# Kernel optimization log

Hardware: AMD Instinct MI355X
Metric: run time of the kernel (lower is better)

## Reference

```python
import jax, jax.numpy as jnp
import numpy as np

Q_DEFAULT = 8
XI_MAX = 0.4          # center frequency of the highest-frequency wavelet (cycles/sample)
BW_RATIO = 0.8        # bandwidth-to-center-frequency ratio
LOG_EPS = 1e-6


def _make_filters(T, Q):
    """Morlet-style analytic filter bank in the Fourier domain (all static numpy)."""
    J = int(np.floor(np.log2(T / 2)))
    freqs = np.fft.fftfreq(T).astype(np.float32)          # [T], in [-0.5, 0.5)
    # first-order wavelets: J*Q filters, geometrically spaced, quality factor Q
    n1 = J * Q
    xi1 = (XI_MAX * 2.0 ** (-np.arange(n1) / Q)).astype(np.float32)
    sig1 = (BW_RATIO * xi1 / Q).astype(np.float32)
    psi1 = np.exp(-(freqs[None, :] - xi1[:, None]) ** 2 / (2.0 * sig1[:, None] ** 2)).astype(np.float32)  # [n1, T]
    # second-order wavelets: Q2 = 1, one per octave
    xi2 = (XI_MAX * 2.0 ** (-np.arange(J))).astype(np.float32)
    sig2 = (BW_RATIO * xi2).astype(np.float32)
    psi2 = np.exp(-(freqs[None, :] - xi2[:, None]) ** 2 / (2.0 * sig2[:, None] ** 2)).astype(np.float32)  # [J, T]
    # low-pass (phi): Gaussian at scale 2^J
    sigma_phi = np.float32(BW_RATIO * XI_MAX * 2.0 ** (-J))
    phi = np.exp(-(freqs ** 2) / (2.0 * sigma_phi ** 2)).astype(np.float32)  # [T]
    # valid second-order paths: xi2 strictly below xi1 (frequency-decreasing cascade)
    pair_j1, pair_k = [], []
    for k in range(J):
        for j1 in range(n1):
            if xi2[k] < xi1[j1]:
                pair_j1.append(j1)
                pair_k.append(k)
    return psi1, psi2, phi, np.asarray(pair_j1, np.int32), np.asarray(pair_k, np.int32)


def _scatter(x_flat, psi1, psi2, phi, pair_j1, pair_k):
    """x_flat: [N, T] real. Returns S: [N, 1 + n1 + n_pairs, T]."""
    xh = jnp.fft.fft(x_flat)                                   # [N, T] complex
    S0 = jnp.fft.ifft(xh * phi).real[:, None, :]               # order 0 (dropped later)
    U1 = jnp.abs(jnp.fft.ifft(xh[:, None, :] * psi1[None]))    # [N, n1, T]
    U1h = jnp.fft.fft(U1)
    S1 = jnp.fft.ifft(U1h * phi).real                          # [N, n1, T]
    U2 = jnp.abs(jnp.fft.ifft(U1h[:, pair_j1, :] * psi2[pair_k][None]))  # [N, P, T]
    S2 = jnp.fft.ifft(jnp.fft.fft(U2) * phi).real              # [N, P, T]
    return jnp.concatenate([S0, S1, S2], axis=1)


def setup_inputs() -> dict:
    key = jax.random.key(0)
    x = jax.random.normal(key, (8, 2048, 6), dtype=jnp.float32)
    return {"x": x}


def reference(x):
    B, T, C = x.shape
    psi1, psi2, phi, pj, pk = _make_filters(T, Q_DEFAULT)
    psi1, psi2, phi = jnp.asarray(psi1), jnp.asarray(psi2), jnp.asarray(phi)
    # vectorize the original per-channel Python loop: fold channels into batch
    xf = jnp.transpose(x, (0, 2, 1)).reshape(B * C, T)          # [B*C, T]
    S = _scatter(xf, psi1, psi2, phi, pj, pk)                   # [B*C, n_coef+1, T]
    out = jnp.mean(jnp.log(S[:, 1:, :] + LOG_EPS), axis=-1)     # drop order-0, log, time-mean
    return out.reshape(B, C, -1).transpose(0, 2, 1)             # [B, n_coef, C]
```

## Files before the change

kernel.cpp:

```cpp
#include <hip/hip_runtime.h>

#define NTH 256
#define U1H_STRIDE 21504

#define PHI1 0.29504296f
#define PHI2 0.0075683594f
#define GCUT 18.0f

__device__ __forceinline__ int swz(int i) { return i ^ (((i >> 4) & 3) * 5); }

__device__ __forceinline__ float2 cmul(float2 a, float2 b) {
  return make_float2(a.x * b.x - a.y * b.y, a.x * b.y + a.y * b.x);
}

template <int W>
__device__ __forceinline__ float wsum(float v) {
#pragma unroll
  for (int off = 1; off < W; off <<= 1) v += __shfl_xor(v, off, 64);
  return v;
}

template <int M>
__device__ __forceinline__ int prevM(int i) {
  if (M == 128)
    return ((i >> 5) & 3) | (((i >> 3) & 3) << 2) | (((i >> 1) & 3) << 4) | ((i & 1) << 6);
  else if (M == 256)
    return ((i & 3) << 6) | (((i >> 2) & 3) << 4) | (((i >> 4) & 3) << 2) | ((i >> 6) & 3);
  else if (M == 512)
    return ((i >> 7) & 3) | (((i >> 5) & 3) << 2) | (((i >> 3) & 3) << 4) |
           (((i >> 1) & 3) << 6) | ((i & 1) << 8);
  else if (M == 1024)
    return ((i >> 8) & 3) | (((i >> 6) & 3) << 2) | (((i >> 4) & 3) << 4) |
           (((i >> 2) & 3) << 6) | ((i & 3) << 8);
  else
    return ((i >> 9) & 3) | (((i >> 7) & 3) << 2) | (((i >> 5) & 3) << 4) |
           (((i >> 3) & 3) << 6) | (((i >> 1) & 3) << 8) | ((i & 1) << 10);
}

template <bool INV>
__device__ __forceinline__ void dif4(float2* A, int j, int ls, float astep) {
  const int s = 1 << ls;
  const int e = j & (s - 1);
  const int base = ((j >> ls) << (ls + 2)) | e;
  float2 w1;
  __sincosf(astep * (float)e, &w1.y, &w1.x);
  if (INV) w1.y = -w1.y;
  const float2 w2 = cmul(w1, w1);
  const float2 w3 = cmul(w2, w1);
  const float2 a0 = A[swz(base)];
  const float2 a1 = A[swz(base + s)];
  const float2 a2 = A[swz(base + 2 * s)];
  const float2 a3 = A[swz(base + 3 * s)];
  const float t0x = a0.x + a2.x, t0y = a0.y + a2.y;
  const float t1x = a0.x - a2.x, t1y = a0.y - a2.y;
  const float t2x = a1.x + a3.x, t2y = a1.y + a3.y;
  const float bdx = a1.x - a3.x, bdy = a1.y - a3.y;
  const float sgn = INV ? -1.0f : 1.0f;
  const float t3x = sgn * bdy, t3y = -sgn * bdx;
  A[swz(base)]         = make_float2(t0x + t2x, t0y + t2y);
  A[swz(base + s)]     = cmul(make_float2(t1x + t3x, t1y + t3y), w1);
  A[swz(base + 2 * s)] = cmul(make_float2(t0x - t2x, t0y - t2y), w2);
  A[swz(base + 3 * s)] = cmul(make_float2(t1x - t3x, t1y - t3y), w3);
}

__device__ __forceinline__ void dit4(float2* A, int j, int ls, float astep) {
  const int s = 1 << ls;
  const int e = j & (s - 1);
  const int base = ((j >> ls) << (ls + 2)) | e;
  float2 w1;
  __sincosf(astep * (float)e, &w1.y, &w1.x);
  const float2 w2 = cmul(w1, w1);
  const float2 w3 = cmul(w2, w1);
  const float2 c0 = A[swz(base)];
  const float2 c1 = cmul(A[swz(base + s)], w1);
  const float2 c2 = cmul(A[swz(base + 2 * s)], w2);
  const float2 c3 = cmul(A[swz(base + 3 * s)], w3);
  const float t0x = c0.x + c2.x, t0y = c0.y + c2.y;
  const float t1x = c0.x - c2.x, t1y = c0.y - c2.y;
  const float t2x = c1.x + c3.x, t2y = c1.y + c3.y;
  const float bdx = c1.x - c3.x, bdy = c1.y - c3.y;
  const float t3x = bdy, t3y = -bdx;
  A[swz(base)]         = make_float2(t0x + t2x, t0y + t2y);
  A[swz(base + s)]     = make_float2(t1x + t3x, t1y + t3y);
  A[swz(base + 2 * s)] = make_float2(t0x - t2x, t0y - t2y);
  A[swz(base + 3 * s)] = make_float2(t1x - t3x, t1y - t3y);
}

__device__ __forceinline__ void r2pair(float2* A, int g) {
  const float2 a = A[swz(2 * g)];
  const float2 b = A[swz(2 * g + 1)];
  A[swz(2 * g)]     = make_float2(a.x + b.x, a.y + b.y);
  A[swz(2 * g + 1)] = make_float2(a.x - b.x, a.y - b.y);
}

template <int M> struct LMof { static constexpr int v =
  (M == 2048) ? 11 : (M == 1024) ? 10 : (M == 512) ? 9 : (M == 256) ? 8 : 7; };

template <int M, bool INV>
__device__ __forceinline__ void dif_blk(float2* A) {
  constexpr int LM = LMof<M>::v;
  constexpr int NB = M / 4;
  const int tid = (int)threadIdx.x;
#pragma unroll
  for (int ls = LM - 2; ls >= (LM & 1); ls -= 2) {
    const float astep = -1.5707963267948966f / (float)(1 << ls);
    __syncthreads();
#pragma unroll
    for (int i = 0; i < NB / NTH; ++i) dif4<INV>(A, tid + NTH * i, ls, astep);
  }
  if (LM & 1) {
    __syncthreads();
#pragma unroll
    for (int i = 0; i < (M / 2) / NTH; ++i) r2pair(A, tid + NTH * i);
  }
  __syncthreads();
}

template <int M>
__device__ __forceinline__ void dit_blk(float2* A) {
  constexpr int LM = LMof<M>::v;
  constexpr int NB = M / 4;
  const int tid = (int)threadIdx.x;
  if (LM & 1) {
    __syncthreads();
#pragma unroll
    for (int i = 0; i < (M / 2) / NTH; ++i) r2pair(A, tid + NTH * i);
  }
#pragma unroll
  for (int ls = (LM & 1); ls <= LM - 2; ls += 2) {
    const float astep = -1.5707963267948966f / (float)(1 << ls);
    __syncthreads();
#pragma unroll
    for (int i = 0; i < NB / NTH; ++i) dit4(A, tid + NTH * i, ls, astep);
  }
  __syncthreads();
}

template <int M, bool INV, int LANES>
__device__ __forceinline__ void dif_w(float2* Aw, int l) {
  constexpr int LM = LMof<M>::v;
  constexpr int NB = M / 4;
#pragma unroll
  for (int ls = LM - 2; ls >= (LM & 1); ls -= 2) {
    const float astep = -1.5707963267948966f / (float)(1 << ls);
#pragma unroll
    for (int i = 0; i < NB / LANES; ++i) dif4<INV>(Aw, l + LANES * i, ls, astep);
  }
  if (LM & 1) {
#pragma unroll
    for (int i = 0; i < (M / 2) / LANES; ++i) r2pair(Aw, l + LANES * i);
  }
}

template <int M, int LANES>
__device__ __forceinline__ void dit_w(float2* Aw, int l) {
  constexpr int LM = LMof<M>::v;
  constexpr int NB = M / 4;
  if (LM & 1) {
#pragma unroll
    for (int i = 0; i < (M / 2) / LANES; ++i) r2pair(Aw, l + LANES * i);
  }
#pragma unroll
  for (int ls = (LM & 1); ls <= LM - 2; ls += 2) {
    const float astep = -1.5707963267948966f / (float)(1 << ls);
#pragma unroll
    for (int i = 0; i < NB / LANES; ++i) dit4(Aw, l + LANES * i, ls, astep);
  }
}

__device__ __forceinline__ int u1h_off(int j1) {
  const int o = j1 >> 3;
  if (o == 0) return j1 * 1024;
  if (o == 1) return 8192 + (j1 - 8) * 512;
  if (o == 2) return 12288 + (j1 - 16) * 256;
  return 14336 + (j1 - 24) * 128;
}

__global__ __launch_bounds__(NTH) void kA(const float* __restrict__ x,
                                          float2* __restrict__ xh) {
  __shared__ float2 A[2048];
  const int n = blockIdx.x, b = n / 6, c = n % 6;
  const float* xp = x + (size_t)b * (2048 * 6) + c;
#pragma unroll
  for (int i = 0; i < 8; ++i) {
    const int t = (int)threadIdx.x + NTH * i;
    A[swz(t)] = make_float2(xp[t * 6], 0.0f);
  }
  dif_blk<2048, false>(A);
#pragma unroll
  for (int i = 0; i < 8; ++i) {
    const int t = (int)threadIdx.x + NTH * i;
    xh[(size_t)n * 2048 + prevM<2048>(t)] = A[swz(t)];
  }
}

template <int M1>
__device__ __forceinline__ void kB_blk(float2* A, const float2* __restrict__ src,
                                       float2* __restrict__ U1h, float* __restrict__ out,
                                       int n, int b, int c, int j1) {
  constexpr int F = 2048 / M1;
  constexpr int NR = M1 / NTH;
  const int tid = (int)threadIdx.x;
  const float xi = 0.4f * exp2f(-0.125f * (float)j1);
  const float sig = 0.1f * xi;
  const float i2s = 1.0f / (2.0f * sig * sig);
#pragma unroll
  for (int i = 0; i < NR; ++i) {
    const int m = tid + NTH * i;
    float2 acc = make_float2(0.0f, 0.0f);
#pragma unroll
    for (int q = 0; q < F; ++q) {
      const int f = m + q * M1;
      const float fr = (float)(f < 1024 ? f : f - 2048) * (1.0f / 2048.0f);
      const float d = fr - xi;
      const float dd = d * d * i2s;
      if (dd < GCUT) {
        const float g = __expf(-dd);
        const float2 v = src[f];
        acc.x += v.x * g; acc.y += v.y * g;
      }
    }
    A[swz(m)] = acc;
  }
  dif_blk<M1, true>(A);
#pragma unroll
  for (int i = 0; i < NR; ++i) {
    const int m = tid + NTH * i;
    const float2 zv = A[swz(m)];
    A[swz(m)] = make_float2(sqrtf(zv.x * zv.x + zv.y * zv.y) * (1.0f / 2048.0f), 0.0f);
  }
  dit_blk<M1>(A);
  float2* dst = U1h + (size_t)n * U1H_STRIDE + u1h_off(j1);
#pragma unroll
  for (int i = 0; i < NR; ++i) {
    const int m = tid + NTH * i;
    dst[m] = A[swz(m)];
  }
  const float invM = 1.0f / (float)M1;
  const float c0 = A[0].x * invM;
  const float2 U1 = A[1], U2 = A[2];
  __syncthreads();
  const float k1 = PHI1 * 2.0f * invM, k2 = PHI2 * 2.0f * invM;
  float part = 0.0f;
#pragma unroll
  for (int i = 0; i < NR; ++i) {
    const int t = tid + NTH * i;
    float sv, cv;
    __sincosf((6.283185307179586f / (float)M1) * (float)t, &sv, &cv);
    float acc = c0 + k1 * (U1.x * cv - U1.y * sv);
    const float c2 = cv * cv - sv * sv, s2 = 2.0f * sv * cv;
    acc += k2 * (U2.x * c2 - U2.y * s2);
    part += __logf(acc + 1e-6f);
  }
  part = wsum<64>(part);
  float* scr = (float*)A;
  const int lane = tid & 63, wid = tid >> 6;
  if (lane == 0) scr[wid] = part;
  __syncthreads();
  if (tid == 0)
    out[((size_t)b * 440 + j1) * 6 + c] = (scr[0] + scr[1] + scr[2] + scr[3]) * invM;
}

template <int M1>
__device__ __forceinline__ void kB_wav(float2* A, const float2* __restrict__ src,
                                       float2* __restrict__ U1h, float* __restrict__ out,
                                       int n, int b, int c, int j1base) {
  constexpr int NRW = M1 / 64;
  constexpr int F = 2048 / M1;
  const int tid = (int)threadIdx.x;
  const int l = tid & 63, wid = tid >> 6;
  const int j1 = j1base + wid;
  float2* Aw = A + wid * M1;
  const float xi = 0.4f * exp2f(-0.125f * (float)j1);
  const float sig = 0.1f * xi;
  const float i2s = 1.0f / (2.0f * sig * sig);
#pragma unroll
  for (int i = 0; i < NRW; ++i) {
    const int m = l + 64 * i;
    float2 acc = make_float2(0.0f, 0.0f);
#pragma unroll
    for (int q = 0; q < F; ++q) {
      const int f = m + q * M1;
      const float fr = (float)(f < 1024 ? f : f - 2048) * (1.0f / 2048.0f);
      const float d = fr - xi;
      const float dd = d * d * i2s;
      if (dd < GCUT) {
        const float g = __expf(-dd);
        const float2 v = src[f];
        acc.x += v.x * g; acc.y += v.y * g;
      }
    }
    Aw[swz(m)] = acc;
  }
  dif_w<M1, true, 64>(Aw, l);
#pragma unroll
  for (int i = 0; i < NRW; ++i) {
    const int m = l + 64 * i;
    const float2 zv = Aw[swz(m)];
    Aw[swz(m)] = make_float2(sqrtf(zv.x * zv.x + zv.y * zv.y) * (1.0f / 2048.0f), 0.0f);
  }
  dit_w<M1, 64>(Aw, l);
  float2* dst = U1h + (size_t)n * U1H_STRIDE + u1h_off(j1);
#pragma unroll
  for (int i = 0; i < NRW; ++i) {
    const int m = l + 64 * i;
    dst[m] = Aw[swz(m)];
  }
  const float invM = 1.0f / (float)M1;
  const float c0 = Aw[0].x * invM;
  const float2 U1 = Aw[1], U2 = Aw[2];
  const float k1 = PHI1 * 2.0f * invM, k2 = PHI2 * 2.0f * invM;
  float part = 0.0f;
#pragma unroll
  for (int i = 0; i < NRW; ++i) {
    const int t = l + 64 * i;
    float sv, cv;
    __sincosf((6.283185307179586f / (float)M1) * (float)t, &sv, &cv);
    float acc = c0 + k1 * (U1.x * cv - U1.y * sv);
    const float c2 = cv * cv - sv * sv, s2 = 2.0f * sv * cv;
    acc += k2 * (U2.x * c2 - U2.y * s2);
    part += __logf(acc + 1e-6f);
  }
  part = wsum<64>(part);
  if (l == 0) out[((size_t)b * 440 + j1) * 6 + c] = part * invM;
}

__device__ __forceinline__ void kB_dual(float2* A, const float2* __restrict__ src,
                                        float2* __restrict__ U1h, float* __restrict__ out,
                                        int n, int b, int c, int j1base) {
  const int tid = (int)threadIdx.x;
  const int l = tid & 63, wid = tid >> 6;
  const int h = l >> 5, ll = l & 31;
  const int j1 = j1base + 2 * wid + h;
  float2* Ah = A + wid * 256 + h * 128;
  const float xi = 0.4f * exp2f(-0.125f * (float)j1);
  const float sig = 0.1f * xi;
  const float i2s = 1.0f / (2.0f * sig * sig);
#pragma unroll
  for (int i = 0; i < 4; ++i) {
    const int m = ll + 32 * i;
    float2 acc = make_float2(0.0f, 0.0f);
#pragma unroll
    for (int q = 0; q < 16; ++q) {
      const int f = m + q * 128;
      const float fr = (float)(f < 1024 ? f : f - 2048) * (1.0f / 2048.0f);
      const float d = fr - xi;
      const float dd = d * d * i2s;
      if (dd < GCUT) {
        const float g = __expf(-dd);
        const float2 v = src[f];
        acc.x += v.x * g; acc.y += v.y * g;
      }
    }
    Ah[swz(m)] = acc;
  }
  dif_w<128, true, 32>(Ah, ll);
#pragma unroll
  for (int i = 0; i < 4; ++i) {
    const int m = ll + 32 * i;
    const float2 zv = Ah[swz(m)];
    Ah[swz(m)] = make_float2(sqrtf(zv.x * zv.x + zv.y * zv.y) * (1.0f / 2048.0f), 0.0f);
  }
  dit_w<128, 32>(Ah, ll);
  float2* dst = U1h + (size_t)n * U1H_STRIDE + u1h_off(j1);
#pragma unroll
  for (int i = 0; i < 4; ++i) {
    const int m = ll + 32 * i;
    dst[m] = Ah[swz(m)];
  }
  const float invM = 1.0f / 128.0f;
  const float c0 = Ah[0].x * invM;
  const float2 U1 = Ah[1], U2 = Ah[2];
  const float k1 = PHI1 * 2.0f * invM, k2 = PHI2 * 2.0f * invM;
  float part = 0.0f;
#pragma unroll
  for (int i = 0; i < 4; ++i) {
    const int t = ll + 32 * i;
    float sv, cv;
    __sincosf((6.283185307179586f / 128.0f) * (float)t, &sv, &cv);
    float acc = c0 + k1 * (U1.x * cv - U1.y * sv);
    const float c2 = cv * cv - sv * sv, s2 = 2.0f * sv * cv;
    acc += k2 * (U2.x * c2 - U2.y * s2);
    part += __logf(acc + 1e-6f);
  }
  part = wsum<32>(part);
  if (ll == 0) out[((size_t)b * 440 + j1) * 6 + c] = part * invM;
}

__global__ __launch_bounds__(NTH, 8) void kB_all(const float2* __restrict__ xh,
                                                 float2* __restrict__ U1h,
                                                 float* __restrict__ out) {
  __shared__ float2 A[2048];
  const int ci = (int)blockIdx.x / 48;
  const int n  = (int)blockIdx.x % 48;
  const int b = n / 6, c = n % 6;
  const float2* src = xh + (size_t)n * 2048;
  if (ci < 2)       kB_wav<512>(A, src, U1h, out, n, b, c, 8 + 4 * ci);
  else if (ci < 10) kB_blk<1024>(A, src, U1h, out, n, b, c, ci - 2);
  else if (ci < 12) kB_wav<256>(A, src, U1h, out, n, b, c, 16 + 4 * (ci - 10));
  else              kB_dual(A, src, U1h, out, n, b, c, 24 + 8 * (ci - 12));
}

template <int M2>
__device__ __forceinline__ void kC_blk(float2* A, const float2* __restrict__ V,
                                       float* __restrict__ outp, int M1, int F, float xi) {
  constexpr int NR2 = M2 / NTH;
  const int tid = (int)threadIdx.x;
  const float sg = 0.8f * xi;
  const float i2s = 1.0f / (2.0f * sg * sg);
#pragma unroll
  for (int ii = 0; ii < NR2; ++ii) {
    const int m = tid + NTH * ii;
    float2 acc = make_float2(0.0f, 0.0f);
    for (int q = 0; q < F; ++q) {
      const int f = m + q * M2;
      const float fr = (float)(f < (M1 >> 1) ? f : f - M1) * (1.0f / 2048.0f);
      const float d = fr - xi;
      const float dd = d * d * i2s;
      if (dd < GCUT) {
        const float g = __expf(-dd);
        const float2 vv = V[f];
        acc.x += vv.x * g; acc.y += vv.y * g;
      }
    }
    A[swz(m)] = acc;
  }
  dif_blk<M2, true>(A);
  const float invM1f = 1.0f / (float)M1;
  float b0 = 0, b1r = 0, b1i = 0, b2r = 0, b2i = 0;
#pragma unroll
  for (int ii = 0; ii < NR2; ++ii) {
    const int idx = tid + NTH * ii;
    const float2 zv = A[swz(idx)];
    const float u = sqrtf(zv.x * zv.x + zv.y * zv.y) * invM1f;
    const int t = prevM<M2>(idx);
    float sv, cv;
    __sincosf((6.283185307179586f / (float)M2) * (float)t, &sv, &cv);
    b0 += u;
    b1r += u * cv; b1i -= u * sv;
    const float c2 = cv * cv - sv * sv, s2 = 2.0f * sv * cv;
    b2r += u * c2; b2i -= u * s2;
  }
  b0 = wsum<64>(b0);
  b1r = wsum<64>(b1r); b1i = wsum<64>(b1i);
  b2r = wsum<64>(b2r); b2i = wsum<64>(b2i);
  __syncthreads();
  float* scr = (float*)A;
  const int lane = tid & 63, wid = tid >> 6;
  if (lane == 0) {
    scr[wid * 5 + 0] = b0;
    scr[wid * 5 + 1] = b1r; scr[wid * 5 + 2] = b1i;
    scr[wid * 5 + 3] = b2r; scr[wid * 5 + 4] = b2i;
  }
  __syncthreads();
  float Bv[5];
#pragma unroll
  for (int bi = 0; bi < 5; ++bi)
    Bv[bi] = scr[bi] + scr[5 + bi] + scr[10 + bi] + scr[15 + bi];
  const float k1 = 2.0f * PHI1, k2 = 2.0f * PHI2;
  const float invM2 = 1.0f / (float)M2;
  float part = 0.0f;
#pragma unroll
  for (int ii = 0; ii < NR2; ++ii) {
    const int idx = tid + NTH * ii;
    const int t = prevM<M2>(idx);
    float sv, cv;
    __sincosf((6.283185307179586f / (float)M2) * (float)t, &sv, &cv);
    float acc = Bv[0] + k1 * (Bv[1] * cv - Bv[2] * sv);
    const float c2 = cv * cv - sv * sv, s2 = 2.0f * sv * cv;
    acc += k2 * (Bv[3] * c2 - Bv[4] * s2);
    part += __logf(acc * invM2 + 1e-6f);
  }
  part = wsum<64>(part);
  if (lane == 0) scr[20 + wid] = part;
  __syncthreads();
  if (tid == 0)
    *outp = (scr[20] + scr[21] + scr[22] + scr[23]) * invM2;
}

template <int M2>
__device__ __forceinline__ void kC_wav(float2* Aw, const float2* __restrict__ V,
                                       float* __restrict__ outp, int M1, int F,
                                       float xi, int l) {
  constexpr int NR2 = M2 / 64;
  const float sg = 0.8f * xi;
  const float i2s = 1.0f / (2.0f * sg * sg);
#pragma unroll
  for (int ii = 0; ii < NR2; ++ii) {
    const int m = l + 64 * ii;
    float2 acc = make_float2(0.0f, 0.0f);
    for (int q = 0; q < F; ++q) {
      const int f = m + q * M2;
      const float fr = (float)(f < (M1 >> 1) ? f : f - M1) * (1.0f / 2048.0f);
      const float d = fr - xi;
      const float dd = d * d * i2s;
      if (dd < GCUT) {
        const float g = __expf(-dd);
        const float2 vv = V[f];
        acc.x += vv.x * g; acc.y += vv.y * g;
      }
    }
    Aw[swz(m)] = acc;
  }
  dif_w<M2, true, 64>(Aw, l);
  const float invM1f = 1.0f / (float)M1;
  float cvs[NR2], svs[NR2];
  float b0 = 0, b1r = 0, b1i = 0, b2r = 0, b2i = 0;
#pragma unroll
  for (int ii = 0; ii < NR2; ++ii) {
    const int idx = l + 64 * ii;
    const float2 zv = Aw[swz(idx)];
    const float u = sqrtf(zv.x * zv.x + zv.y * zv.y) * invM1f;
    const int t = prevM<M2>(idx);
    float sv, cv;
    __sincosf((6.283185307179586f / (float)M2) * (float)t, &sv, &cv);
    cvs[ii] = cv; svs[ii] = sv;
    b0 += u;
    b1r += u * cv; b1i -= u * sv;
    const float c2 = cv * cv - sv * sv, s2 = 2.0f * sv * cv;
    b2r += u * c2; b2i -= u * s2;
  }
  b0 = wsum<64>(b0);
  b1r = wsum<64>(b1r); b1i = wsum<64>(b1i);
  b2r = wsum<64>(b2r); b2i = wsum<64>(b2i);
  const float k1 = 2.0f * PHI1, k2 = 2.0f * PHI2;
  const float invM2 = 1.0f / (float)M2;
  float part = 0.0f;
#pragma unroll
  for (int ii = 0; ii < NR2; ++ii) {
    const float cv = cvs[ii], sv = svs[ii];
    float acc = b0 + k1 * (b1r * cv - b1i * sv);
    const float c2 = cv * cv - sv * sv, s2 = 2.0f * sv * cv;
    acc += k2 * (b2r * c2 - b2i * s2);
    part += __logf(acc * invM2 + 1e-6f);
  }
  part = wsum<64>(part);
  if (l == 0) *outp = part * invM2;
}

__device__ __forceinline__ void kC_dual(float2* Ah, const float2* __restrict__ V,
                                        float* __restrict__ outp, int M1, int F,
                                        float xi, int ll) {
  const float sg = 0.8f * xi;
  const float i2s = 1.0f / (2.0f * sg * sg);
#pragma unroll
  for (int ii = 0; ii < 4; ++ii) {
    const int m = ll + 32 * ii;
    float2 acc = make_float2(0.0f, 0.0f);
    for (int q = 0; q < F; ++q) {
      const int f = m + q * 128;
      const float fr = (float)(f < (M1 >> 1) ? f : f - M1) * (1.0f / 2048.0f);
      const float d = fr - xi;
      const float dd = d * d * i2s;
      if (dd < GCUT) {
        const float g = __expf(-dd);
        const float2 vv = V[f];
        acc.x += vv.x * g; acc.y += vv.y * g;
      }
    }
    Ah[swz(m)] = acc;
  }
  dif_w<128, true, 32>(Ah, ll);
  const float invM1f = 1.0f / (float)M1;
  float cvs[4], svs[4];
  float b0 = 0, b1r = 0, b1i = 0, b2r = 0, b2i = 0;
#pragma unroll
  for (int ii = 0; ii < 4; ++ii) {
    const int idx = ll + 32 * ii;
    const float2 zv = Ah[swz(idx)];
    const float u = sqrtf(zv.x * zv.x + zv.y * zv.y) * invM1f;
    const int t = prevM<128>(idx);
    float sv, cv;
    __sincosf((6.283185307179586f / 128.0f) * (float)t, &sv, &cv);
    cvs[ii] = cv; svs[ii] = sv;
    b0 += u;
    b1r += u * cv; b1i -= u * sv;
    const float c2 = cv * cv - sv * sv, s2 = 2.0f * sv * cv;
    b2r += u * c2; b2i -= u * s2;
  }
  b0 = wsum<32>(b0);
  b1r = wsum<32>(b1r); b1i = wsum<32>(b1i);
  b2r = wsum<32>(b2r); b2i = wsum<32>(b2i);
  const float k1 = 2.0f * PHI1, k2 = 2.0f * PHI2;
  const float invM2 = 1.0f / 128.0f;
  float part = 0.0f;
#pragma unroll
  for (int ii = 0; ii < 4; ++ii) {
    const float cv = cvs[ii], sv = svs[ii];
    float acc = b0 + k1 * (b1r * cv - b1i * sv);
    const float c2 = cv * cv - sv * sv, s2 = 2.0f * sv * cv;
    acc += k2 * (b2r * c2 - b2i * s2);
    part += __logf(acc * invM2 + 1e-6f);
  }
  part = wsum<32>(part);
  if (ll == 0) *outp = part * invM2;
}

__global__ __launch_bounds__(NTH, 8) void kC_all(const float2* __restrict__ U1h,
                                                 float* __restrict__ out) {
  __shared__ float2 A[2048];
  const int ci = (int)blockIdx.x / 48;
  const int n  = (int)blockIdx.x % 48;
  const int b = n / 6, c = n % 6;
  const float2* base = U1h + (size_t)n * U1H_STRIDE;
  const int wid = (int)threadIdx.x >> 6;
  const int l = (int)threadIdx.x & 63;
  if (ci < 4) {
    const int k = 2;
    const int j1 = 4 * ci + wid;
    const int M1 = (j1 < 8) ? 1024 : 512;
    const float xi = 0.4f * exp2f(-(float)k);
    const int p = 4 * k * (k - 1) + j1;
    kC_wav<512>(A + wid * 512, base + u1h_off(j1),
                out + ((size_t)b * 440 + 80 + p) * 6 + c, M1, M1 / 512, xi, l);
  } else if (ci < 6) {
    const int k = 3;
    const int j1 = 4 * (ci - 4) + wid;
    const float xi = 0.4f * exp2f(-(float)k);
    const int p = 4 * k * (k - 1) + j1;
    kC_wav<512>(A + wid * 512, base + u1h_off(j1),
                out + ((size_t)b * 440 + 80 + p) * 6 + c, 1024, 2, xi, l);
  } else if (ci < 14) {
    const int k = 1;
    const int j1 = ci - 6;
    const float xi = 0.4f * exp2f(-(float)k);
    const int p = 4 * k * (k - 1) + j1;
    kC_blk<1024>(A, base + u1h_off(j1), out + ((size_t)b * 440 + 80 + p) * 6 + c,
                 1024, 1, xi);
  } else if (ci < 18) {
    const int k = 3;
    const int j1 = 8 + 4 * (ci - 14) + wid;
    const int M1 = (j1 < 16) ? 512 : 256;
    const float xi = 0.4f * exp2f(-(float)k);
    const int p = 4 * k * (k - 1) + j1;
    kC_wav<256>(A + wid * 256, base + u1h_off(j1),
                out + ((size_t)b * 440 + 80 + p) * 6 + c, M1, M1 / 256, xi, l);
  } else if (ci < 20) {
    const int k = 4;
    const int j1 = 4 * (ci - 18) + wid;
    const float xi = 0.4f * exp2f(-(float)k);
    const int p = 4 * k * (k - 1) + j1;
    kC_wav<256>(A + wid * 256, base + u1h_off(j1),
                out + ((size_t)b * 440 + 80 + p) * 6 + c, 1024, 4, xi, l);
  } else if (ci < 23) {
    const int k = 4;
    const int h = l >> 5, ll = l & 31;
    const int j1 = 8 + 8 * (ci - 20) + 2 * wid + h;
    const int o = j1 >> 3;
    const int M1 = (o < 3) ? (1024 >> o) : 128;
    const float xi = 0.4f * exp2f(-(float)k);
    const int p = 4 * k * (k - 1) + j1;
    kC_dual(A + wid * 256 + h * 128, base + u1h_off(j1),
            out + ((size_t)b * 440 + 80 + p) * 6 + c, M1, M1 / 128, xi, ll);
  } else {
    int g = ci - 23;
    int k = 5;
    while (g >= k) { g -= k; ++k; }
    const int h = l >> 5, ll = l & 31;
    const int j1 = 8 * g + 2 * wid + h;
    const int M1 = (g < 3) ? (1024 >> g) : 128;
    const float xi = 0.4f * exp2f(-(float)k);
    const int p = 4 * k * (k - 1) + j1;
    kC_dual(A + wid * 256 + h * 128, base + u1h_off(j1),
            out + ((size_t)b * 440 + 80 + p) * 6 + c, M1, M1 / 128, xi, ll);
  }
}

extern "C" void kernel_launch(void* const* d_in, const int* in_sizes, int n_in,
                              void* d_out, int out_size, void* d_ws, size_t ws_size,
                              hipStream_t stream) {
  (void)in_sizes; (void)n_in; (void)out_size; (void)ws_size;
  const float* x = (const float*)d_in[0];
  float* out = (float*)d_out;
  float2* U1h = (float2*)d_ws;
  float2* xh = (float2*)((char*)d_ws + (size_t)48 * U1H_STRIDE * sizeof(float2));
  kA<<<dim3(48), dim3(NTH), 0, stream>>>(x, xh);
  kB_all<<<dim3(19 * 48), dim3(NTH), 0, stream>>>(xh, U1h, out);
  kC_all<<<dim3(58 * 48), dim3(NTH), 0, stream>>>(U1h, out);
}
```

Measured before the change: 96.70 us.

## Fuse first- and second-order scattering kernels, keep U1 spectrum in LDS

Merges the first-order (kB) and second-order (kC) kernels into one kernel. Each block computes a parent first-order wavelet spectrum in shared memory and then evaluates all of its descendant second-order paths directly from that shared-memory copy. This removes the global U1h workspace round trip and one kernel launch. In exchange the per-block shared-memory footprint doubles, launch bounds drop to 4 blocks per CU, the grid shrinks from 58*48 to 19*48 blocks, and per-block work becomes uneven. Parallelism and load balance may suffer.

```diff
diff --git a/kernel.cpp b/kernel.cpp
--- a/kernel.cpp
+++ b/kernel.cpp
@@ -1,7 +1,6 @@
 #include <hip/hip_runtime.h>
 
 #define NTH 256
-#define U1H_STRIDE 21504
 
 #define PHI1 0.29504296f
 #define PHI2 0.0075683594f
@@ -168,14 +167,6 @@
   }
 }
 
-__device__ __forceinline__ int u1h_off(int j1) {
-  const int o = j1 >> 3;
-  if (o == 0) return j1 * 1024;
-  if (o == 1) return 8192 + (j1 - 8) * 512;
-  if (o == 2) return 12288 + (j1 - 16) * 256;
-  return 14336 + (j1 - 24) * 128;
-}
-
 __global__ __launch_bounds__(NTH) void kA(const float* __restrict__ x,
                                           float2* __restrict__ xh) {
   __shared__ float2 A[2048];
@@ -194,12 +185,13 @@
   }
 }
 
-template <int M1>
-__device__ __forceinline__ void kB_blk(float2* A, const float2* __restrict__ src,
-                                       float2* __restrict__ U1h, float* __restrict__ out,
-                                       int n, int b, int c, int j1) {
-  constexpr int F = 2048 / M1;
-  constexpr int NR = M1 / NTH;
+
+__device__ __forceinline__ void parent_blk1024(float2* A, float* scr,
+                                               const float2* __restrict__ src,
+                                               float* __restrict__ out,
+                                               int b, int c, int j1) {
+  constexpr int M1 = 1024;
+  constexpr int NR = 4;
   const int tid = (int)threadIdx.x;
   const float xi = 0.4f * exp2f(-0.125f * (float)j1);
   const float sig = 0.1f * xi;
@@ -207,6 +199,64 @@
 #pragma unroll
   for (int i = 0; i < NR; ++i) {
     const int m = tid + NTH * i;
+    float2 acc = make_float2(0.0f, 0.0f);
+#pragma unroll
+    for (int q = 0; q < 2; ++q) {
+      const int f = m + q * M1;
+      const float fr = (float)(f < 1024 ? f : f - 2048) * (1.0f / 2048.0f);
+      const float d = fr - xi;
+      const float dd = d * d * i2s;
+      if (dd < GCUT) {
+        const float g = __expf(-dd);
+        const float2 v = src[f];
+        acc.x += v.x * g; acc.y += v.y * g;
+      }
+    }
+    A[swz(m)] = acc;
+  }
+  dif_blk<M1, true>(A);
+#pragma unroll
+  for (int i = 0; i < NR; ++i) {
+    const int m = tid + NTH * i;
+    const float2 zv = A[swz(m)];
+    A[swz(m)] = make_float2(sqrtf(zv.x * zv.x + zv.y * zv.y) * (1.0f / 2048.0f), 0.0f);
+  }
+  dit_blk<M1>(A);
+  const float invM = 1.0f / (float)M1;
+  const float c0 = A[0].x * invM;
+  const float2 U1 = A[1], U2 = A[2];
+  const float k1 = PHI1 * 2.0f * invM, k2 = PHI2 * 2.0f * invM;
+  float part = 0.0f;
+#pragma unroll
+  for (int i = 0; i < NR; ++i) {
+    const int t = tid + NTH * i;
+    float sv, cv;
+    __sincosf((6.283185307179586f / (float)M1) * (float)t, &sv, &cv);
+    float acc = c0 + k1 * (U1.x * cv - U1.y * sv);
+    const float c2 = cv * cv - sv * sv, s2 = 2.0f * sv * cv;
+    acc += k2 * (U2.x * c2 - U2.y * s2);
+    part += __logf(acc + 1e-6f);
+  }
+  part = wsum<64>(part);
+  const int lane = tid & 63, wid = tid >> 6;
+  if (lane == 0) scr[wid] = part;
+  __syncthreads();
+  if (tid == 0)
+    out[((size_t)b * 440 + j1) * 6 + c] = (scr[0] + scr[1] + scr[2] + scr[3]) * invM;
+}
+
+template <int M1>
+__device__ __forceinline__ void parent_wav(float2* Aw, const float2* __restrict__ src,
+                                           float* __restrict__ out,
+                                           int b, int c, int j1, int l) {
+  constexpr int NRW = M1 / 64;
+  constexpr int F = 2048 / M1;
+  const float xi = 0.4f * exp2f(-0.125f * (float)j1);
+  const float sig = 0.1f * xi;
+  const float i2s = 1.0f / (2.0f * sig * sig);
+#pragma unroll
+  for (int i = 0; i < NRW; ++i) {
+    const int m = l + 64 * i;
     float2 acc = make_float2(0.0f, 0.0f);
 #pragma unroll
     for (int q = 0; q < F; ++q) {
@@ -220,76 +270,6 @@
         acc.x += v.x * g; acc.y += v.y * g;
       }
     }
-    A[swz(m)] = acc;
-  }
-  dif_blk<M1, true>(A);
-#pragma unroll
-  for (int i = 0; i < NR; ++i) {
-    const int m = tid + NTH * i;
-    const float2 zv = A[swz(m)];
-    A[swz(m)] = make_float2(sqrtf(zv.x * zv.x + zv.y * zv.y) * (1.0f / 2048.0f), 0.0f);
-  }
-  dit_blk<M1>(A);
-  float2* dst = U1h + (size_t)n * U1H_STRIDE + u1h_off(j1);
-#pragma unroll
-  for (int i = 0; i < NR; ++i) {
-    const int m = tid + NTH * i;
-    dst[m] = A[swz(m)];
-  }
-  const float invM = 1.0f / (float)M1;
-  const float c0 = A[0].x * invM;
-  const float2 U1 = A[1], U2 = A[2];
-  __syncthreads();
-  const float k1 = PHI1 * 2.0f * invM, k2 = PHI2 * 2.0f * invM;
-  float part = 0.0f;
-#pragma unroll
-  for (int i = 0; i < NR; ++i) {
-    const int t = tid + NTH * i;
-    float sv, cv;
-    __sincosf((6.283185307179586f / (float)M1) * (float)t, &sv, &cv);
-    float acc = c0 + k1 * (U1.x * cv - U1.y * sv);
-    const float c2 = cv * cv - sv * sv, s2 = 2.0f * sv * cv;
-    acc += k2 * (U2.x * c2 - U2.y * s2);
-    part += __logf(acc + 1e-6f);
-  }
-  part = wsum<64>(part);
-  float* scr = (float*)A;
-  const int lane = tid & 63, wid = tid >> 6;
-  if (lane == 0) scr[wid] = part;
-  __syncthreads();
-  if (tid == 0)
-    out[((size_t)b * 440 + j1) * 6 + c] = (scr[0] + scr[1] + scr[2] + scr[3]) * invM;
-}
-
-template <int M1>
-__device__ __forceinline__ void kB_wav(float2* A, const float2* __restrict__ src,
-                                       float2* __restrict__ U1h, float* __restrict__ out,
-                                       int n, int b, int c, int j1base) {
-  constexpr int NRW = M1 / 64;
-  constexpr int F = 2048 / M1;
-  const int tid = (int)threadIdx.x;
-  const int l = tid & 63, wid = tid >> 6;
-  const int j1 = j1base + wid;
-  float2* Aw = A + wid * M1;
-  const float xi = 0.4f * exp2f(-0.125f * (float)j1);
-  const float sig = 0.1f * xi;
-  const float i2s = 1.0f / (2.0f * sig * sig);
-#pragma unroll
-  for (int i = 0; i < NRW; ++i) {
-    const int m = l + 64 * i;
-    float2 acc = make_float2(0.0f, 0.0f);
-#pragma unroll
-    for (int q = 0; q < F; ++q) {
-      const int f = m + q * M1;
-      const float fr = (float)(f < 1024 ? f : f - 2048) * (1.0f / 2048.0f);
-      const float d = fr - xi;
-      const float dd = d * d * i2s;
-      if (dd < GCUT) {
-        const float g = __expf(-dd);
-        const float2 v = src[f];
-        acc.x += v.x * g; acc.y += v.y * g;
-      }
-    }
     Aw[swz(m)] = acc;
   }
   dif_w<M1, true, 64>(Aw, l);
@@ -300,12 +280,6 @@
     Aw[swz(m)] = make_float2(sqrtf(zv.x * zv.x + zv.y * zv.y) * (1.0f / 2048.0f), 0.0f);
   }
   dit_w<M1, 64>(Aw, l);
-  float2* dst = U1h + (size_t)n * U1H_STRIDE + u1h_off(j1);
-#pragma unroll
-  for (int i = 0; i < NRW; ++i) {
-    const int m = l + 64 * i;
-    dst[m] = Aw[swz(m)];
-  }
   const float invM = 1.0f / (float)M1;
   const float c0 = Aw[0].x * invM;
   const float2 U1 = Aw[1], U2 = Aw[2];
@@ -325,14 +299,9 @@
   if (l == 0) out[((size_t)b * 440 + j1) * 6 + c] = part * invM;
 }
 
-__device__ __forceinline__ void kB_dual(float2* A, const float2* __restrict__ src,
-                                        float2* __restrict__ U1h, float* __restrict__ out,
-                                        int n, int b, int c, int j1base) {
-  const int tid = (int)threadIdx.x;
-  const int l = tid & 63, wid = tid >> 6;
-  const int h = l >> 5, ll = l & 31;
-  const int j1 = j1base + 2 * wid + h;
-  float2* Ah = A + wid * 256 + h * 128;
+__device__ __forceinline__ void parent_dual(float2* Ah, const float2* __restrict__ src,
+                                            float* __restrict__ out,
+                                            int b, int c, int j1, int ll) {
   const float xi = 0.4f * exp2f(-0.125f * (float)j1);
   const float sig = 0.1f * xi;
   const float i2s = 1.0f / (2.0f * sig * sig);
@@ -362,12 +331,6 @@
     Ah[swz(m)] = make_float2(sqrtf(zv.x * zv.x + zv.y * zv.y) * (1.0f / 2048.0f), 0.0f);
   }
   dit_w<128, 32>(Ah, ll);
-  float2* dst = U1h + (size_t)n * U1H_STRIDE + u1h_off(j1);
-#pragma unroll
-  for (int i = 0; i < 4; ++i) {
-    const int m = ll + 32 * i;
-    dst[m] = Ah[swz(m)];
-  }
   const float invM = 1.0f / 128.0f;
   const float c0 = Ah[0].x * invM;
   const float2 U1 = Ah[1], U2 = Ah[2];
@@ -387,101 +350,10 @@
   if (ll == 0) out[((size_t)b * 440 + j1) * 6 + c] = part * invM;
 }
 
-__global__ __launch_bounds__(NTH, 8) void kB_all(const float2* __restrict__ xh,
-                                                 float2* __restrict__ U1h,
-                                                 float* __restrict__ out) {
-  __shared__ float2 A[2048];
-  const int ci = (int)blockIdx.x / 48;
-  const int n  = (int)blockIdx.x % 48;
-  const int b = n / 6, c = n % 6;
-  const float2* src = xh + (size_t)n * 2048;
-  if (ci < 2)       kB_wav<512>(A, src, U1h, out, n, b, c, 8 + 4 * ci);
-  else if (ci < 10) kB_blk<1024>(A, src, U1h, out, n, b, c, ci - 2);
-  else if (ci < 12) kB_wav<256>(A, src, U1h, out, n, b, c, 16 + 4 * (ci - 10));
-  else              kB_dual(A, src, U1h, out, n, b, c, 24 + 8 * (ci - 12));
-}
-
 template <int M2>
-__device__ __forceinline__ void kC_blk(float2* A, const float2* __restrict__ V,
-                                       float* __restrict__ outp, int M1, int F, float xi) {
-  constexpr int NR2 = M2 / NTH;
-  const int tid = (int)threadIdx.x;
-  const float sg = 0.8f * xi;
-  const float i2s = 1.0f / (2.0f * sg * sg);
-#pragma unroll
-  for (int ii = 0; ii < NR2; ++ii) {
-    const int m = tid + NTH * ii;
-    float2 acc = make_float2(0.0f, 0.0f);
-    for (int q = 0; q < F; ++q) {
-      const int f = m + q * M2;
-      const float fr = (float)(f < (M1 >> 1) ? f : f - M1) * (1.0f / 2048.0f);
-      const float d = fr - xi;
-      const float dd = d * d * i2s;
-      if (dd < GCUT) {
-        const float g = __expf(-dd);
-        const float2 vv = V[f];
-        acc.x += vv.x * g; acc.y += vv.y * g;
-      }
-    }
-    A[swz(m)] = acc;
-  }
-  dif_blk<M2, true>(A);
-  const float invM1f = 1.0f / (float)M1;
-  float b0 = 0, b1r = 0, b1i = 0, b2r = 0, b2i = 0;
-#pragma unroll
-  for (int ii = 0; ii < NR2; ++ii) {
-    const int idx = tid + NTH * ii;
-    const float2 zv = A[swz(idx)];
-    const float u = sqrtf(zv.x * zv.x + zv.y * zv.y) * invM1f;
-    const int t = prevM<M2>(idx);
-    float sv, cv;
-    __sincosf((6.283185307179586f / (float)M2) * (float)t, &sv, &cv);
-    b0 += u;
-    b1r += u * cv; b1i -= u * sv;
-    const float c2 = cv * cv - sv * sv, s2 = 2.0f * sv * cv;
-    b2r += u * c2; b2i -= u * s2;
-  }
-  b0 = wsum<64>(b0);
-  b1r = wsum<64>(b1r); b1i = wsum<64>(b1i);
-  b2r = wsum<64>(b2r); b2i = wsum<64>(b2i);
-  __syncthreads();
-  float* scr = (float*)A;
-  const int lane = tid & 63, wid = tid >> 6;
-  if (lane == 0) {
-    scr[wid * 5 + 0] = b0;
-    scr[wid * 5 + 1] = b1r; scr[wid * 5 + 2] = b1i;
-    scr[wid * 5 + 3] = b2r; scr[wid * 5 + 4] = b2i;
-  }
-  __syncthreads();
-  float Bv[5];
-#pragma unroll
-  for (int bi = 0; bi < 5; ++bi)
-    Bv[bi] = scr[bi] + scr[5 + bi] + scr[10 + bi] + scr[15 + bi];
-  const float k1 = 2.0f * PHI1, k2 = 2.0f * PHI2;
-  const float invM2 = 1.0f / (float)M2;
-  float part = 0.0f;
-#pragma unroll
-  for (int ii = 0; ii < NR2; ++ii) {
-    const int idx = tid + NTH * ii;
-    const int t = prevM<M2>(idx);
-    float sv, cv;
-    __sincosf((6.283185307179586f / (float)M2) * (float)t, &sv, &cv);
-    float acc = Bv[0] + k1 * (Bv[1] * cv - Bv[2] * sv);
-    const float c2 = cv * cv - sv * sv, s2 = 2.0f * sv * cv;
-    acc += k2 * (Bv[3] * c2 - Bv[4] * s2);
-    part += __logf(acc * invM2 + 1e-6f);
-  }
-  part = wsum<64>(part);
-  if (lane == 0) scr[20 + wid] = part;
-  __syncthreads();
-  if (tid == 0)
-    *outp = (scr[20] + scr[21] + scr[22] + scr[23]) * invM2;
-}
-
-template <int M2>
-__device__ __forceinline__ void kC_wav(float2* Aw, const float2* __restrict__ V,
-                                       float* __restrict__ outp, int M1, int F,
-                                       float xi, int l) {
+__device__ __forceinline__ void desc_wav(float2* Aw, const float2* __restrict__ Vl,
+                                         float* __restrict__ outp, int M1, int F,
+                                         float xi, int l) {
   constexpr int NR2 = M2 / 64;
   const float sg = 0.8f * xi;
   const float i2s = 1.0f / (2.0f * sg * sg);
@@ -496,7 +368,7 @@
       const float dd = d * d * i2s;
       if (dd < GCUT) {
         const float g = __expf(-dd);
-        const float2 vv = V[f];
+        const float2 vv = Vl[swz(f)];
         acc.x += vv.x * g; acc.y += vv.y * g;
       }
     }
@@ -538,9 +410,9 @@
   if (l == 0) *outp = part * invM2;
 }
 
-__device__ __forceinline__ void kC_dual(float2* Ah, const float2* __restrict__ V,
-                                        float* __restrict__ outp, int M1, int F,
-                                        float xi, int ll) {
+__device__ __forceinline__ void desc_dual(float2* Ah, const float2* __restrict__ Vl,
+                                          float* __restrict__ outp, int M1, int F,
+                                          float xi, int ll) {
   const float sg = 0.8f * xi;
   const float i2s = 1.0f / (2.0f * sg * sg);
 #pragma unroll
@@ -554,7 +426,7 @@
       const float dd = d * d * i2s;
       if (dd < GCUT) {
         const float g = __expf(-dd);
-        const float2 vv = V[f];
+        const float2 vv = Vl[swz(f)];
         acc.x += vv.x * g; acc.y += vv.y * g;
       }
     }
@@ -596,73 +468,72 @@
   if (ll == 0) *outp = part * invM2;
 }
 
-__global__ __launch_bounds__(NTH, 8) void kC_all(const float2* __restrict__ U1h,
-                                                 float* __restrict__ out) {
-  __shared__ float2 A[2048];
+__device__ __forceinline__ float* o2p(float* out, int b, int c, int j1, int k) {
+  return out + ((size_t)b * 440 + 80 + 4 * k * (k - 1) + j1) * 6 + c;
+}
+__device__ __forceinline__ float xi2f(int k) { return 0.4f * exp2f(-(float)k); }
+
+__global__ __launch_bounds__(NTH, 4) void kBC(const float2* __restrict__ xh,
+                                              float* __restrict__ out) {
+  __shared__ float2 L[4096];
   const int ci = (int)blockIdx.x / 48;
   const int n  = (int)blockIdx.x % 48;
   const int b = n / 6, c = n % 6;
-  const float2* base = U1h + (size_t)n * U1H_STRIDE;
-  const int wid = (int)threadIdx.x >> 6;
-  const int l = (int)threadIdx.x & 63;
-  if (ci < 4) {
-    const int k = 2;
-    const int j1 = 4 * ci + wid;
-    const int M1 = (j1 < 8) ? 1024 : 512;
-    const float xi = 0.4f * exp2f(-(float)k);
-    const int p = 4 * k * (k - 1) + j1;
-    kC_wav<512>(A + wid * 512, base + u1h_off(j1),
-                out + ((size_t)b * 440 + 80 + p) * 6 + c, M1, M1 / 512, xi, l);
-  } else if (ci < 6) {
-    const int k = 3;
-    const int j1 = 4 * (ci - 4) + wid;
-    const float xi = 0.4f * exp2f(-(float)k);
-    const int p = 4 * k * (k - 1) + j1;
-    kC_wav<512>(A + wid * 512, base + u1h_off(j1),
-                out + ((size_t)b * 440 + 80 + p) * 6 + c, 1024, 2, xi, l);
-  } else if (ci < 14) {
-    const int k = 1;
-    const int j1 = ci - 6;
-    const float xi = 0.4f * exp2f(-(float)k);
-    const int p = 4 * k * (k - 1) + j1;
-    kC_blk<1024>(A, base + u1h_off(j1), out + ((size_t)b * 440 + 80 + p) * 6 + c,
-                 1024, 1, xi);
-  } else if (ci < 18) {
-    const int k = 3;
-    const int j1 = 8 + 4 * (ci - 14) + wid;
-    const int M1 = (j1 < 16) ? 512 : 256;
-    const float xi = 0.4f * exp2f(-(float)k);
-    const int p = 4 * k * (k - 1) + j1;
-    kC_wav<256>(A + wid * 256, base + u1h_off(j1),
-                out + ((size_t)b * 440 + 80 + p) * 6 + c, M1, M1 / 256, xi, l);
-  } else if (ci < 20) {
-    const int k = 4;
-    const int j1 = 4 * (ci - 18) + wid;
-    const float xi = 0.4f * exp2f(-(float)k);
-    const int p = 4 * k * (k - 1) + j1;
-    kC_wav<256>(A + wid * 256, base + u1h_off(j1),
-                out + ((size_t)b * 440 + 80 + p) * 6 + c, 1024, 4, xi, l);
-  } else if (ci < 23) {
-    const int k = 4;
-    const int h = l >> 5, ll = l & 31;
-    const int j1 = 8 + 8 * (ci - 20) + 2 * wid + h;
-    const int o = j1 >> 3;
-    const int M1 = (o < 3) ? (1024 >> o) : 128;
-    const float xi = 0.4f * exp2f(-(float)k);
-    const int p = 4 * k * (k - 1) + j1;
-    kC_dual(A + wid * 256 + h * 128, base + u1h_off(j1),
-            out + ((size_t)b * 440 + 80 + p) * 6 + c, M1, M1 / 128, xi, ll);
+  const float2* src = xh + (size_t)n * 2048;
+  const int tid = (int)threadIdx.x;
+  const int wid = tid >> 6, l = tid & 63;
+  const int h = l >> 5, ll = l & 31;
+
+  if (ci < 2) {
+    const int j1 = 8 + 4 * ci + wid;
+    float2* Aw = L + wid * 1024;
+    float2* W  = Aw + 512;
+    parent_wav<512>(Aw, src, out, b, c, j1, l);
+    desc_wav<512>(W, Aw, o2p(out, b, c, j1, 2), 512, 1, xi2f(2), l);
+    desc_wav<256>(W, Aw, o2p(out, b, c, j1, 3), 512, 2, xi2f(3), l);
+    float2* Wh = W + h * 128;
+    for (int i = 0; i < 3; ++i) {
+      const int k = 4 + 2 * i + h;
+      desc_dual(Wh, Aw, o2p(out, b, c, j1, k), 512, 4, xi2f(k), ll);
+    }
+  } else if (ci < 4) {
+    const int j1 = 16 + 4 * (ci - 2) + wid;
+    float2* Aw = L + wid * 512;
+    float2* W  = Aw + 256;
+    parent_wav<256>(Aw, src, out, b, c, j1, l);
+    desc_wav<256>(W, Aw, o2p(out, b, c, j1, 3), 256, 1, xi2f(3), l);
+    float2* Wh = W + h * 128;
+    for (int i = 0; i < 3; ++i) {
+      const int k = 4 + 2 * i + h;
+      desc_dual(Wh, Aw, o2p(out, b, c, j1, k), 256, 2, xi2f(k), ll);
+    }
+  } else if (ci < 12) {
+    const int j1 = ci - 4;
+    float* scr = (float*)(L + 3968);
+    parent_blk1024(L, scr, src, out, b, c, j1);
+    if (wid == 0) {
+      desc_wav<1024>(L + 1024, L, o2p(out, b, c, j1, 1), 1024, 1, xi2f(1), l);
+    } else if (wid == 1) {
+      desc_wav<512>(L + 2048, L, o2p(out, b, c, j1, 2), 1024, 2, xi2f(2), l);
+      const int k = 5 + h;
+      desc_dual(L + 3328 + h * 128, L, o2p(out, b, c, j1, k), 1024, 8, xi2f(k), ll);
+    } else if (wid == 2) {
+      desc_wav<512>(L + 2560, L, o2p(out, b, c, j1, 3), 1024, 2, xi2f(3), l);
+      const int k = 7 + h;
+      desc_dual(L + 3584 + h * 128, L, o2p(out, b, c, j1, k), 1024, 8, xi2f(k), ll);
+    } else {
+      desc_wav<256>(L + 3072, L, o2p(out, b, c, j1, 4), 1024, 4, xi2f(4), l);
+      if (h == 0)
+        desc_dual(L + 3840, L, o2p(out, b, c, j1, 9), 1024, 8, xi2f(9), ll);
+    }
   } else {
-    int g = ci - 23;
-    int k = 5;
-    while (g >= k) { g -= k; ++k; }
-    const int h = l >> 5, ll = l & 31;
-    const int j1 = 8 * g + 2 * wid + h;
-    const int M1 = (g < 3) ? (1024 >> g) : 128;
-    const float xi = 0.4f * exp2f(-(float)k);
-    const int p = 4 * k * (k - 1) + j1;
-    kC_dual(A + wid * 256 + h * 128, base + u1h_off(j1),
-            out + ((size_t)b * 440 + 80 + p) * 6 + c, M1, M1 / 128, xi, ll);
+    const int o = ci - 9;
+    const int j1 = 8 * o + 2 * wid + h;
+    float2* Ah = L + (2 * wid + h) * 256;
+    parent_dual(Ah, src, out, b, c, j1, ll);
+    float2* W = Ah + 128;
+    for (int k = o + 1; k <= 9; ++k)
+      desc_dual(W, Ah, o2p(out, b, c, j1, k), 128, 1, xi2f(k), ll);
   }
 }
 
@@ -672,9 +543,7 @@
   (void)in_sizes; (void)n_in; (void)out_size; (void)ws_size;
   const float* x = (const float*)d_in[0];
   float* out = (float*)d_out;
-  float2* U1h = (float2*)d_ws;
-  float2* xh = (float2*)((char*)d_ws + (size_t)48 * U1H_STRIDE * sizeof(float2));
+  float2* xh = (float2*)d_ws;
   kA<<<dim3(48), dim3(NTH), 0, stream>>>(x, xh);
-  kB_all<<<dim3(19 * 48), dim3(NTH), 0, stream>>>(xh, U1h, out);
-  kC_all<<<dim3(58 * 48), dim3(NTH), 0, stream>>>(U1h, out);
-}
+  kBC<<<dim3(19 * 48), dim3(NTH), 0, stream>>>(xh, out);
+}
```

After: 87.03 us. -10.0%, faster.
